# Kernel optimization log

Measured on AMD Instinct MI355X. Metric: run time of the kernel, lower is better.

## Reference

```python
import jax, jax.numpy as jnp
import numpy as np

B, S, D, H, DK, DV = 4, 2048, 1024, 16, 64, 64

def setup_inputs() -> dict:
    key = jax.random.key(0)
    ks = jax.random.split(key, 7)
    scale = 0.02
    queries = jax.random.normal(ks[0], (B, S, D), jnp.float32)
    keys_ = jax.random.normal(ks[1], (B, S, D), jnp.float32)
    values = jax.random.normal(ks[2], (B, S, D), jnp.float32)
    # causal mask: 1 where attendable, 0 where masked
    mask = jnp.tril(jnp.ones((S, S), jnp.int32))[None, None, :, :]
    W_Q = jax.random.normal(ks[3], (D, H * DK), jnp.float32) * scale
    W_K = jax.random.normal(ks[4], (D, H * DK), jnp.float32) * scale
    W_V = jax.random.normal(ks[5], (D, H * DV), jnp.float32) * scale
    W_O = jax.random.normal(ks[6], (H * DV, D), jnp.float32) * scale
    return {"queries": queries, "keys": keys_, "values": values, "mask": mask,
            "W_Q": W_Q, "W_K": W_K, "W_V": W_V, "W_O": W_O}

def reference(queries, keys, values, mask, W_Q, W_K, W_V, W_O):
    b, skv, _ = keys.shape
    sq = queries.shape[1]
    scaling = 1.0 / (DK ** 0.5)
    Q = (queries @ W_Q).reshape(b, sq, H, DK)   # [B,Sq,H,DK]
    K = (keys @ W_K).reshape(b, skv, H, DK)     # [B,Skv,H,DK]
    V = (values @ W_V).reshape(b, skv, H, DV)   # [B,Skv,H,DV]
    scores = jnp.einsum('bqhd,bkhd->bhqk', Q, K)
    scores = jnp.where(mask == 0, -jnp.inf, scores)
    probs = jax.nn.softmax(scores * scaling, axis=-1)
    attn = jnp.einsum('bhqk,bkhd->bqhd', probs, V).reshape(b, sq, H * DV)
    return attn @ W_O
```

## Files before the change

kernel.cpp:

```cpp
#include <hip/hip_runtime.h>
#include <hip/hip_bf16.h>


typedef __attribute__((ext_vector_type(8))) __bf16 bf16x8;
typedef __attribute__((ext_vector_type(8))) unsigned short ushort8v;
typedef __attribute__((ext_vector_type(4))) unsigned short ushort4v;
typedef __attribute__((ext_vector_type(4))) unsigned uint4v;
typedef __attribute__((ext_vector_type(2))) unsigned uint2v;
typedef __attribute__((ext_vector_type(4))) float float4v;

#define MFMA16(a, b, c) __builtin_amdgcn_mfma_f32_16x16x32_bf16((a), (b), (c), 0, 0, 0)
#define GLDS16(g, l)                                                     \
    __builtin_amdgcn_global_load_lds(                                    \
        (const __attribute__((address_space(1))) void*)(g),              \
        (__attribute__((address_space(3))) void*)(l), 16, 0, 0)

__device__ __forceinline__ unsigned short f2bf(float f) {
    union { float f; unsigned u; } v; v.f = f;
    unsigned r = v.u + 0x7fffu + ((v.u >> 16) & 1u);
    return (unsigned short)(r >> 16);
}
__device__ __forceinline__ unsigned pkbf(float a, float b) {
    union { float f; unsigned u; } x, y; x.f = a; y.f = b;
    return __builtin_amdgcn_perm(y.u + 0x8000u, x.u + 0x8000u, 0x07060302u);
}
__device__ __forceinline__ float exp2_fast(float x) {
#if __has_builtin(__builtin_amdgcn_exp2f)
    return __builtin_amdgcn_exp2f(x);
#else
    return __builtin_exp2f(x);
#endif
}

__global__ __launch_bounds__(256) void cvt_bf16(
    const float* __restrict__ X, unsigned short* __restrict__ Y)
{
    size_t i = ((size_t)blockIdx.x * 256 + threadIdx.x) * 8;
    float4v a = *(const float4v*)&X[i];
    float4v b = *(const float4v*)&X[i + 4];
    uint4v o = { pkbf(a.x, a.y), pkbf(a.z, a.w), pkbf(b.x, b.y), pkbf(b.z, b.w) };
    *(uint4v*)&Y[i] = o;
}

__global__ __launch_bounds__(256) void transpose_w(
    const float* __restrict__ W, unsigned short* __restrict__ Wt, float scale)
{
    __shared__ unsigned short T[64][72];
    const int t = threadIdx.x;
    const int n0 = blockIdx.x * 64, k0 = blockIdx.y * 64;
    for (int i = 0; i < 4; i++) {
        int idx = i * 256 + t, r = idx >> 4, c = (idx & 15) * 4;
        float4v v = *(const float4v*)&W[(size_t)(k0 + r) * 1024 + n0 + c];
        T[c + 0][r] = f2bf(v.x * scale); T[c + 1][r] = f2bf(v.y * scale);
        T[c + 2][r] = f2bf(v.z * scale); T[c + 3][r] = f2bf(v.w * scale);
    }
    __syncthreads();
    for (int i = 0; i < 4; i++) {
        int idx = i * 256 + t, r = idx >> 4, c = (idx & 15) * 4;
        ushort4v o; o.x = T[r][c]; o.y = T[r][c + 1]; o.z = T[r][c + 2]; o.w = T[r][c + 3];
        *(ushort4v*)&Wt[(size_t)(n0 + r) * 1024 + k0 + c] = o;
    }
}

template <bool OUT_BF16>
__global__ __launch_bounds__(256) void gemm_bb(
    const unsigned short* __restrict__ A, const unsigned short* __restrict__ Bt,
    void* __restrict__ Cp, int M, int N, int K)
{
    __shared__ unsigned short As[128 * 64];
    __shared__ unsigned short Bs[128 * 64];

    const int t = threadIdx.x;
    const int lane = t & 63, w = t >> 6;
    const int lanelo = lane & 15, quad = lane >> 4;
    const int wm = w >> 1, wn = w & 1;
    const int m0 = blockIdx.y * 128, n0 = blockIdx.x * 128;

    float4v acc[4][4];
    for (int i = 0; i < 4; i++)
        for (int j = 0; j < 4; j++) acc[i][j] = (float4v)(0.f);

    for (int k0 = 0; k0 < K; k0 += 64) {
        for (int i = 0; i < 4; i++) {
            int idx = i * 256 + t, row = idx >> 3, ch = idx & 7;
            GLDS16(A + (size_t)(m0 + row) * K + k0 + ch * 8, &As[idx * 8]);
        }
        for (int i = 0; i < 4; i++) {
            int idx = i * 256 + t, row = idx >> 3, ch = idx & 7;
            GLDS16(Bt + (size_t)(n0 + row) * K + k0 + ch * 8, &Bs[idx * 8]);
        }
        __syncthreads();
        for (int ks = 0; ks < 2; ks++) {
            bf16x8 af[4], bfr[4];
            for (int mi = 0; mi < 4; mi++)
                af[mi] = *(const bf16x8*)&As[(wm * 64 + mi * 16 + lanelo) * 64 + ks * 32 + quad * 8];
            for (int ni = 0; ni < 4; ni++)
                bfr[ni] = *(const bf16x8*)&Bs[(wn * 64 + ni * 16 + lanelo) * 64 + ks * 32 + quad * 8];
            for (int mi = 0; mi < 4; mi++)
                for (int ni = 0; ni < 4; ni++)
                    acc[mi][ni] = MFMA16(af[mi], bfr[ni], acc[mi][ni]);
        }
        __syncthreads();
    }

    for (int mi = 0; mi < 4; mi++)
        for (int ni = 0; ni < 4; ni++) {
            int col = n0 + wn * 64 + ni * 16 + lanelo;
            for (int r = 0; r < 4; r++) {
                int row = m0 + wm * 64 + mi * 16 + quad * 4 + r;
                float v = acc[mi][ni][r];
                if constexpr (OUT_BF16)
                    ((unsigned short*)Cp)[(size_t)row * N + col] = f2bf(v);
                else
                    ((float*)Cp)[(size_t)row * N + col] = v;
            }
        }
}

__global__ __launch_bounds__(256, 4) void attn_k(
    const unsigned short* __restrict__ Qb, const unsigned short* __restrict__ Kb,
    const unsigned short* __restrict__ Vt, unsigned short* __restrict__ Ob)
{
    __shared__ __align__(16) unsigned short Ks[2][64 * 64];
    __shared__ __align__(16) unsigned short Vs[2][64 * 64];
    __shared__ __align__(16) unsigned short Ps[4][16 * 64];

    const int t = threadIdx.x;
    const int lane = t & 63, w = t >> 6;
    const int lanelo = lane & 15, quad = lane >> 4;
    const int bh = blockIdx.x;
    const int b = bh >> 4, h = bh & 15;

    unsigned short* pw = &Ps[w][0];
    const int rsw = (lanelo & 7) * 8;
    const int l7 = lanelo & 7;

    auto stage = [&](int buf, int kt) {
        for (int i = 0; i < 2; i++) {
            int idx = i * 256 + t, row = idx >> 3, ch = idx & 7;
            GLDS16(Kb + ((size_t)(b * 2048 + kt * 64 + row)) * 1024 + h * 64
                       + ((ch ^ (row & 7)) << 3),
                   &Ks[buf][idx * 8]);
        }
        for (int i = 0; i < 2; i++) {
            int idx = i * 256 + t, row = idx >> 3, ch = idx & 7;
            GLDS16(Vt + (size_t)(h * 64 + row) * 8192 + b * 2048 + kt * 64
                       + ((ch ^ (row & 7)) << 3),
                   &Vs[buf][idx * 8]);
        }
    };

    for (int half = 0; half < 2; half++) {
        const int qt = half ? blockIdx.y : 31 - blockIdx.y;
        const int qb = qt * 64;
        const int nkt = qt + 1;
        const int q = qb + w * 16 + lanelo;

        bf16x8 qf[2];
        {
            const unsigned short* qp = Qb + ((size_t)(b * 2048) + q) * 1024 + h * 64 + quad * 8;
            qf[0] = *(const bf16x8*)(qp);
            qf[1] = *(const bf16x8*)(qp + 32);
        }
        float4v o[4];
        for (int i = 0; i < 4; i++) o[i] = (float4v)(0.f);
        float m_ = -__builtin_inff(), l_ = 0.f;

        stage(0, 0);
        __syncthreads();

        int cur = 0;
        for (int kt = 0; kt < nkt; kt++) {
            if (kt + 1 < nkt) stage(cur ^ 1, kt + 1);

            const unsigned short* ks = &Ks[cur][0];
            const unsigned short* vs = &Vs[cur][0];

            float4v sc[4];
            for (int nt = 0; nt < 4; nt++) {
                sc[nt] = (float4v)(0.f);
                for (int c = 0; c < 2; c++) {
                    bf16x8 kf = *(const bf16x8*)
                        &ks[(nt * 16 + lanelo) * 64 + ((c * 32 + quad * 8) ^ rsw)];
                    sc[nt] = MFMA16(kf, qf[c], sc[nt]);
                }
            }
            if (kt == nkt - 1) {
                const int kb0 = qb + quad * 4;
                for (int nt = 0; nt < 4; nt++)
                    for (int r = 0; r < 4; r++)
                        if (kb0 + nt * 16 + r > q) sc[nt][r] = -__builtin_inff();
            }
            float mx = sc[0][0];
            for (int nt = 0; nt < 4; nt++)
                for (int r = 0; r < 4; r++) mx = fmaxf(mx, sc[nt][r]);
            mx = fmaxf(mx, __shfl_xor(mx, 16, 64));
            mx = fmaxf(mx, __shfl_xor(mx, 32, 64));
            if (!__all(mx <= m_ + 8.f)) {
                float mnew = fmaxf(m_, mx);
                float alpha = exp2_fast(m_ - mnew);
                l_ *= alpha;
                for (int vt = 0; vt < 4; vt++)
                    for (int r = 0; r < 4; r++) o[vt][r] *= alpha;
                m_ = mnew;
            }
            float rs = 0.f;
            for (int nt = 0; nt < 4; nt++)
                for (int r = 0; r < 4; r++) {
                    float e = exp2_fast(sc[nt][r] - m_);
                    sc[nt][r] = e; rs += e;
                }
            rs += __shfl_xor(rs, 16, 64);
            rs += __shfl_xor(rs, 32, 64);
            l_ += rs;

            for (int nt = 0; nt < 4; nt++) {
                uint2v pv;
                pv.x = pkbf(sc[nt][0], sc[nt][1]);
                pv.y = pkbf(sc[nt][2], sc[nt][3]);
                *(uint2v*)((char*)pw + lanelo * 128
                           + ((((nt << 1) | (quad >> 1)) ^ l7) << 4)
                           + ((quad & 1) << 3)) = pv;
            }
            asm volatile("s_waitcnt lgkmcnt(0)" ::: "memory");
            __builtin_amdgcn_sched_barrier(0);
            for (int c = 0; c < 2; c++) {
                bf16x8 pf = *(const bf16x8*)((const char*)pw + lanelo * 128
                                             + (((c * 4 + quad) ^ l7) << 4));
                for (int vt = 0; vt < 4; vt++) {
                    bf16x8 vf = *(const bf16x8*)
                        &vs[(vt * 16 + lanelo) * 64 + ((c * 32 + quad * 8) ^ rsw)];
                    o[vt] = MFMA16(vf, pf, o[vt]);
                }
            }
            __syncthreads();
            cur ^= 1;
        }

        float inv = 1.0f / l_;
        for (int vt = 0; vt < 4; vt++) {
            uint2v ov;
            ov.x = pkbf(o[vt][0] * inv, o[vt][1] * inv);
            ov.y = pkbf(o[vt][2] * inv, o[vt][3] * inv);
            *(uint2v*)((char*)pw + lanelo * 128
                       + ((((vt << 1) | (quad >> 1)) ^ l7) << 4)
                       + ((quad & 1) << 3)) = ov;
        }
        asm volatile("s_waitcnt lgkmcnt(0)" ::: "memory");
        __builtin_amdgcn_sched_barrier(0);
        for (int i = 0; i < 2; i++) {
            int qr = i * 8 + (lane >> 3);
            int ch = lane & 7;
            ushort8v ov = *(const ushort8v*)((const char*)pw + qr * 128
                                             + ((ch ^ (qr & 7)) << 4));
            *(ushort8v*)(Ob + ((size_t)(b * 2048) + qb + w * 16 + qr) * 1024
                         + h * 64 + ch * 8) = ov;
        }
    }
}

extern "C" void kernel_launch(void* const* d_in, const int* in_sizes, int n_in,
                              void* d_out, int out_size, void* d_ws, size_t ws_size,
                              hipStream_t stream) {
    const float* queries = (const float*)d_in[0];
    const float* keys    = (const float*)d_in[1];
    const float* values  = (const float*)d_in[2];
    const float* W_Q = (const float*)d_in[4];
    const float* W_K = (const float*)d_in[5];
    const float* W_V = (const float*)d_in[6];
    const float* W_O = (const float*)d_in[7];

    const size_t SZ = (size_t)4 * 2048 * 1024;
    const size_t WSZ = (size_t)1024 * 1024;
    unsigned short* X   = (unsigned short*)d_ws;
    unsigned short* Qb  = X + SZ;
    unsigned short* Kb  = Qb + SZ;
    unsigned short* Vt  = Kb + SZ;
    unsigned short* Ab  = X;
    unsigned short* WQt = Vt + SZ;
    unsigned short* WKt = WQt + WSZ;
    unsigned short* WVt = WKt + WSZ;
    unsigned short* WOt = WVt + WSZ;

    dim3 blk(256), tg(16, 16);
    hipLaunchKernelGGL(transpose_w, tg, blk, 0, stream, W_Q, WQt, 1.0f);
    hipLaunchKernelGGL(transpose_w, tg, blk, 0, stream, W_K, WKt, 0.125f * 1.44269504088896f);
    hipLaunchKernelGGL(transpose_w, tg, blk, 0, stream, W_V, WVt, 1.0f);
    hipLaunchKernelGGL(transpose_w, tg, blk, 0, stream, W_O, WOt, 1.0f);

    dim3 cg(4096);
    hipLaunchKernelGGL(cvt_bf16, cg, blk, 0, stream, queries, X);
    hipLaunchKernelGGL((gemm_bb<true>), dim3(8, 64), blk, 0, stream, X, WQt, Qb, 8192, 1024, 1024);
    hipLaunchKernelGGL(cvt_bf16, cg, blk, 0, stream, keys, X);
    hipLaunchKernelGGL((gemm_bb<true>), dim3(8, 64), blk, 0, stream, X, WKt, Kb, 8192, 1024, 1024);
    hipLaunchKernelGGL(cvt_bf16, cg, blk, 0, stream, values, X);
    hipLaunchKernelGGL((gemm_bb<true>), dim3(64, 8), blk, 0, stream, WVt, X, Vt, 1024, 8192, 1024);

    hipLaunchKernelGGL(attn_k, dim3(64, 16), blk, 0, stream, Qb, Kb, Vt, Ab);

    hipLaunchKernelGGL((gemm_bb<false>), dim3(8, 64), blk, 0, stream, Ab, WOt, d_out, 8192, 1024, 1024);
}
```

Measured before the change: 355.3 us.

## Fuse fp32-to-bf16 conversion into a single batched QKV projection GEMM

Drops the separate cvt_bf16 passes and folds the fp32-to-bf16 conversion of the activations into the GEMM's tile loading, so the bf16 activation copies are never written to or read back from global memory. The Q, K and V projections run as one 1536-block launch, and the four weight transposes run as one launch via blockIdx.z. This removes several launches and some intermediate traffic. In exchange, the activation tile load becomes a synchronous register load and convert instead of an async global-to-LDS load, and the fp32 activation tile is re-read by every N-tile block, which doubles the bytes read per tile.

```diff
diff --git a/kernel.cpp b/kernel.cpp
--- a/kernel.cpp
+++ b/kernel.cpp
@@ -32,20 +32,17 @@
 #endif
 }
 
-__global__ __launch_bounds__(256) void cvt_bf16(
-    const float* __restrict__ X, unsigned short* __restrict__ Y)
-{
-    size_t i = ((size_t)blockIdx.x * 256 + threadIdx.x) * 8;
-    float4v a = *(const float4v*)&X[i];
-    float4v b = *(const float4v*)&X[i + 4];
-    uint4v o = { pkbf(a.x, a.y), pkbf(a.z, a.w), pkbf(b.x, b.y), pkbf(b.z, b.w) };
-    *(uint4v*)&Y[i] = o;
-}
-
-__global__ __launch_bounds__(256) void transpose_w(
-    const float* __restrict__ W, unsigned short* __restrict__ Wt, float scale)
+__global__ __launch_bounds__(256) void transpose_w4(
+    const float* __restrict__ W0, const float* __restrict__ W1,
+    const float* __restrict__ W2, const float* __restrict__ W3,
+    unsigned short* __restrict__ T0, unsigned short* __restrict__ T1,
+    unsigned short* __restrict__ T2, unsigned short* __restrict__ T3)
 {
     __shared__ unsigned short T[64][72];
+    const int z = blockIdx.z;
+    const float* W = z == 0 ? W0 : z == 1 ? W1 : z == 2 ? W2 : W3;
+    unsigned short* Wt = z == 0 ? T0 : z == 1 ? T1 : z == 2 ? T2 : T3;
+    const float scale = (z == 1) ? 0.125f * 1.44269504088896f : 1.0f;
     const int t = threadIdx.x;
     const int n0 = blockIdx.x * 64, k0 = blockIdx.y * 64;
     for (int i = 0; i < 4; i++) {
@@ -60,6 +57,82 @@
         ushort4v o; o.x = T[r][c]; o.y = T[r][c + 1]; o.z = T[r][c + 2]; o.w = T[r][c + 3];
         *(ushort4v*)&Wt[(size_t)(n0 + r) * 1024 + k0 + c] = o;
     }
+}
+
+__global__ __launch_bounds__(256) void qkv_gemm(
+    const float* __restrict__ Aq, const float* __restrict__ Ak,
+    const float* __restrict__ Av,
+    const unsigned short* __restrict__ WQt, const unsigned short* __restrict__ WKt,
+    const unsigned short* __restrict__ WVt,
+    unsigned short* __restrict__ Qb, unsigned short* __restrict__ Kb,
+    unsigned short* __restrict__ Vto)
+{
+    __shared__ unsigned short As[128 * 64];
+    __shared__ unsigned short Bs[128 * 64];
+
+    const int t = threadIdx.x;
+    const int lane = t & 63, w = t >> 6;
+    const int lanelo = lane & 15, quad = lane >> 4;
+    const int wm = w >> 1, wn = w & 1;
+
+    const int gid = blockIdx.x;
+    const int group = gid >> 9;
+    const int r = gid & 511;
+    const bool vsw = (group == 2);
+
+    const float* act; const unsigned short* wt; unsigned short* out;
+    if (group == 0)      { act = Aq; wt = WQt; out = Qb; }
+    else if (group == 1) { act = Ak; wt = WKt; out = Kb; }
+    else                 { act = Av; wt = WVt; out = Vto; }
+
+    int m0, n0, ldc;
+    if (!vsw) { m0 = (r >> 3) * 128; n0 = (r & 7) * 128; ldc = 1024; }
+    else      { n0 = (r & 63) * 128; m0 = (r >> 6) * 128; ldc = 8192; }
+    const int act0 = vsw ? n0 : m0;
+    const int wt0  = vsw ? m0 : n0;
+    unsigned short* actS = vsw ? Bs : As;
+    unsigned short* wtS  = vsw ? As : Bs;
+
+    float4v acc[4][4];
+    for (int i = 0; i < 4; i++)
+        for (int j = 0; j < 4; j++) acc[i][j] = (float4v)(0.f);
+
+    for (int k0 = 0; k0 < 1024; k0 += 64) {
+        for (int i = 0; i < 4; i++) {
+            int idx = i * 256 + t, row = idx >> 3, ch = idx & 7;
+            GLDS16(wt + (size_t)(wt0 + row) * 1024 + k0 + ch * 8, &wtS[idx * 8]);
+        }
+        for (int i = 0; i < 4; i++) {
+            int s = i * 256 + t, row = s >> 3, ch = s & 7;
+            const float* ap = act + (size_t)(act0 + row) * 1024 + k0 + ch * 8;
+            float4v x = *(const float4v*)ap;
+            float4v y = *(const float4v*)(ap + 4);
+            uint4v o4 = { pkbf(x.x, x.y), pkbf(x.z, x.w),
+                          pkbf(y.x, y.y), pkbf(y.z, y.w) };
+            *(uint4v*)&actS[row * 64 + ch * 8] = o4;
+        }
+        __syncthreads();
+        for (int ks = 0; ks < 2; ks++) {
+            bf16x8 af[4], bfr[4];
+            for (int mi = 0; mi < 4; mi++)
+                af[mi] = *(const bf16x8*)&As[(wm * 64 + mi * 16 + lanelo) * 64 + ks * 32 + quad * 8];
+            for (int ni = 0; ni < 4; ni++)
+                bfr[ni] = *(const bf16x8*)&Bs[(wn * 64 + ni * 16 + lanelo) * 64 + ks * 32 + quad * 8];
+            for (int mi = 0; mi < 4; mi++)
+                for (int ni = 0; ni < 4; ni++)
+                    acc[mi][ni] = MFMA16(af[mi], bfr[ni], acc[mi][ni]);
+        }
+        __syncthreads();
+    }
+
+    for (int mi = 0; mi < 4; mi++)
+        for (int ni = 0; ni < 4; ni++) {
+            int col = n0 + wn * 64 + ni * 16 + lanelo;
+            for (int rr = 0; rr < 4; rr++) {
+                int row = m0 + wm * 64 + mi * 16 + quad * 4 + rr;
+                out[(size_t)row * ldc + col] = f2bf(acc[mi][ni][rr]);
+            }
+        }
 }
 
 template <bool OUT_BF16>
@@ -272,29 +345,21 @@
 
     const size_t SZ = (size_t)4 * 2048 * 1024;
     const size_t WSZ = (size_t)1024 * 1024;
-    unsigned short* X   = (unsigned short*)d_ws;
-    unsigned short* Qb  = X + SZ;
+    unsigned short* Qb  = (unsigned short*)d_ws;
     unsigned short* Kb  = Qb + SZ;
     unsigned short* Vt  = Kb + SZ;
-    unsigned short* Ab  = X;
-    unsigned short* WQt = Vt + SZ;
+    unsigned short* Ab  = Vt + SZ;
+    unsigned short* WQt = Ab + SZ;
     unsigned short* WKt = WQt + WSZ;
     unsigned short* WVt = WKt + WSZ;
     unsigned short* WOt = WVt + WSZ;
 
-    dim3 blk(256), tg(16, 16);
-    hipLaunchKernelGGL(transpose_w, tg, blk, 0, stream, W_Q, WQt, 1.0f);
-    hipLaunchKernelGGL(transpose_w, tg, blk, 0, stream, W_K, WKt, 0.125f * 1.44269504088896f);
-    hipLaunchKernelGGL(transpose_w, tg, blk, 0, stream, W_V, WVt, 1.0f);
-    hipLaunchKernelGGL(transpose_w, tg, blk, 0, stream, W_O, WOt, 1.0f);
-
-    dim3 cg(4096);
-    hipLaunchKernelGGL(cvt_bf16, cg, blk, 0, stream, queries, X);
-    hipLaunchKernelGGL((gemm_bb<true>), dim3(8, 64), blk, 0, stream, X, WQt, Qb, 8192, 1024, 1024);
-    hipLaunchKernelGGL(cvt_bf16, cg, blk, 0, stream, keys, X);
-    hipLaunchKernelGGL((gemm_bb<true>), dim3(8, 64), blk, 0, stream, X, WKt, Kb, 8192, 1024, 1024);
-    hipLaunchKernelGGL(cvt_bf16, cg, blk, 0, stream, values, X);
-    hipLaunchKernelGGL((gemm_bb<true>), dim3(64, 8), blk, 0, stream, WVt, X, Vt, 1024, 8192, 1024);
+    dim3 blk(256);
+    hipLaunchKernelGGL(transpose_w4, dim3(16, 16, 4), blk, 0, stream,
+                       W_Q, W_K, W_V, W_O, WQt, WKt, WVt, WOt);
+
+    hipLaunchKernelGGL(qkv_gemm, dim3(1536), blk, 0, stream,
+                       queries, keys, values, WQt, WKt, WVt, Qb, Kb, Vt);
 
     hipLaunchKernelGGL(attn_k, dim3(64, 16), blk, 0, stream, Qb, Kb, Vt, Ab);
 
```

Result: faster. 342.0 us (-3.7%).
